# Kernel tuning notes

Measured on AMD Instinct MI355X. Metric: run time of the kernel, lower is better.

The kernel has to match this reference:

```python
import jax, jax.numpy as jnp
import numpy as np

N_NODES, N_EDGES = 1024, 4096
D_NODE, D_EDGE, HEADS, N_CLASSES = 128, 256, 4, 16


def setup_inputs() -> dict:
    key = jax.random.key(0)
    ks = jax.random.split(key, 32)
    def w(i, shape):
        return jax.random.normal(ks[i], shape, dtype=jnp.float32) * 0.02
    inp = {
        'node_features': jax.random.normal(ks[0], (N_NODES, D_NODE), dtype=jnp.float32),
        'edge_features': jax.random.normal(ks[1], (N_EDGES, D_EDGE), dtype=jnp.float32),
        'edge_index': jax.random.randint(ks[2], (2, N_EDGES), 0, N_NODES, dtype=jnp.int32),
    }
    i = 3
    for pre in ('a1', 'a2'):
        for nm, shape in [('Wn', (2 * D_NODE, D_EDGE)), ('Wq', (D_EDGE, D_EDGE)),
                          ('Wk', (D_EDGE, D_EDGE)), ('Wv', (D_EDGE, D_EDGE)), ('Wo', (D_EDGE, D_EDGE))]:
            inp[f'{pre}_{nm}'] = w(i, shape); i += 1
            inp[f'{pre}_b{nm[1:].lower()}'] = jnp.zeros((shape[1],), jnp.float32)
    inp['cls_W1'] = w(i, (D_EDGE, D_EDGE)); i += 1
    inp['cls_b1'] = jnp.zeros((D_EDGE,), jnp.float32)
    inp['cls_W2'] = w(i, (D_EDGE, N_CLASSES)); i += 1
    inp['cls_b2'] = jnp.zeros((N_CLASSES,), jnp.float32)
    return inp


def _edge_adjacency(edge_index):
    # edges adjacent iff they share an endpoint (hops=1). [E,E] bool
    src, dst = edge_index[0], edge_index[1]
    return ((src[:, None] == src[None, :]) | (src[:, None] == dst[None, :]) |
            (dst[:, None] == src[None, :]) | (dst[:, None] == dst[None, :]))


def _edge_attention(ef, nf, edge_index, adj, Wn, bn, Wq, bq, Wk, bk, Wv, bv, Wo, bo):
    src, dst = edge_index[0], edge_index[1]
    # gather endpoint node features and fuse into edge representation
    ctx = jnp.concatenate([nf[src], nf[dst]], axis=-1) @ Wn + bn  # [E, D_EDGE]
    x = ef + ctx
    E, D = x.shape
    hd = D // HEADS
    q = (x @ Wq + bq).reshape(E, HEADS, hd)
    k = (x @ Wk + bk).reshape(E, HEADS, hd)
    v = (x @ Wv + bv).reshape(E, HEADS, hd)
    scores = jnp.einsum('ehd,fhd->hef', q, k) / np.float32(np.sqrt(hd))  # [H,E,E]
    scores = jnp.where(adj[None, :, :], scores, jnp.float32(-1e9))
    attn = jax.nn.softmax(scores, axis=-1)
    out = jnp.einsum('hef,fhd->ehd', attn, v).reshape(E, D)
    return x + out @ Wo + bo


def reference(node_features, edge_features, edge_index,
              a1_Wn, a1_bn, a1_Wq, a1_bq, a1_Wk, a1_bk, a1_Wv, a1_bv, a1_Wo, a1_bo,
              a2_Wn, a2_bn, a2_Wq, a2_bq, a2_Wk, a2_bk, a2_Wv, a2_bv, a2_Wo, a2_bo,
              cls_W1, cls_b1, cls_W2, cls_b2):
    adj = _edge_adjacency(edge_index)
    ef = _edge_attention(edge_features, node_features, edge_index, adj,
                         a1_Wn, a1_bn, a1_Wq, a1_bq, a1_Wk, a1_bk, a1_Wv, a1_bv, a1_Wo, a1_bo)
    ef = _edge_attention(ef, node_features, edge_index, adj,
                         a2_Wn, a2_bn, a2_Wq, a2_bq, a2_Wk, a2_bk, a2_Wv, a2_bv, a2_Wo, a2_bo)
    h = jax.nn.gelu(ef @ cls_W1 + cls_b1, approximate=False)
    return h @ cls_W2 + cls_b2
```

## Files before the change

kernel.cpp:

```cpp
#include <hip/hip_runtime.h>
#include <math.h>

#define E_EDGES 4096
#define N_NODES 1024
#define D_NODE 128
#define D_EDGE 256
#define HEADS 4
#define HD 64
#define N_CLASSES 16
#define CAP 128

typedef __attribute__((ext_vector_type(8))) short short8v;
typedef __attribute__((ext_vector_type(4))) float f32x4;

__device__ __forceinline__ unsigned short f2bf(float f) {
    unsigned u = __float_as_uint(f);
    return (unsigned short)((u + 0x7FFFu + ((u >> 16) & 1u)) >> 16);
}
__device__ __forceinline__ float bf2f(unsigned short b) {
    return __uint_as_float(((unsigned)b) << 16);
}

__device__ __forceinline__ void gload_lds16(const void* g, void* l) {
    __builtin_amdgcn_global_load_lds((const __attribute__((address_space(1))) void*)g,
                                     (__attribute__((address_space(3))) void*)l, 16, 0, 0);
}

__device__ __forceinline__ void xcd_remap(int& bx, int& by)
{
    const int nx = gridDim.x;
    const int lid = blockIdx.x + nx * blockIdx.y;
    const int g = lid & 7, s = lid >> 3;
    const int ppx = gridDim.y >> 3;
    by = g * ppx + s / nx;
    bx = s % nx;
}

__global__ __launch_bounds__(256) void prep(
    const float* W0, const float* W1, const float* W2, const float* W3,
    const float* W4, const float* W5, const float* W6, const float* W7,
    const float* W8, const float* W9, const float* W10,
    short* hiT, short* loT,
    const int* __restrict__ src, const int* __restrict__ dst,
    int* __restrict__ cand, int* __restrict__ ccount)
{
    __shared__ float tl[64][65];
    const int t = threadIdx.x;
    if (blockIdx.x < 176) {
        const float* Ws[11] = {W0, W1, W2, W3, W4, W5, W6, W7, W8, W9, W10};
        const int mat = blockIdx.x >> 4, tile = blockIdx.x & 15;
        const int k0 = (tile >> 2) * 64, n0 = (tile & 3) * 64;
        const float* W = Ws[mat];
#pragma unroll
        for (int p = 0; p < 4; ++p) {
            const int kr = (t >> 4) + p * 16;
            const int nc = (t & 15) * 4;
            *(float4*)&tl[kr][nc] = *(const float4*)&W[(size_t)(k0 + kr) * 256 + n0 + nc];
        }
        __syncthreads();
        const int n = t >> 2, ks = (t & 3) * 16;
        short8v h0, h1, l0, l1;
#pragma unroll
        for (int j = 0; j < 8; ++j) {
            const float x = tl[ks + j][n];
            const unsigned short hb = f2bf(x);
            h0[j] = (short)hb; l0[j] = (short)f2bf(x - bf2f(hb));
        }
#pragma unroll
        for (int j = 0; j < 8; ++j) {
            const float x = tl[ks + 8 + j][n];
            const unsigned short hb = f2bf(x);
            h1[j] = (short)hb; l1[j] = (short)f2bf(x - bf2f(hb));
        }
        short* ho = hiT + (size_t)mat * 65536;
        short* lo = loT + (size_t)mat * 65536;
        *(short8v*)&ho[(size_t)(n0 + n) * 256 + k0 + ks] = h0;
        *(short8v*)&ho[(size_t)(n0 + n) * 256 + k0 + ks + 8] = h1;
        *(short8v*)&lo[(size_t)(n0 + n) * 256 + k0 + ks] = l0;
        *(short8v*)&lo[(size_t)(n0 + n) * 256 + k0 + ks + 8] = l1;
    } else {
        const int w = t >> 6, lane = t & 63;
        const int e = (blockIdx.x - 176) * 4 + w;
        const int a = src[e], b = dst[e];
        int* my = cand + (size_t)e * CAP;
        int base = 0;
        for (int c0 = 0; c0 < E_EDGES; c0 += 64) {
            const int f = c0 + lane;
            const int sf = src[f], df = dst[f];
            const bool adj = (sf == a) | (sf == b) | (df == a) | (df == b);
            const unsigned long long mk = __ballot(adj);
            if (adj) {
                const int pos = base + __popcll(mk & ((1ull << lane) - 1ull));
                if (pos < CAP) my[pos] = f;
            }
            base += __popcll(mk);
        }
        if (lane == 0) ccount[e] = (base < CAP) ? base : CAP;
    }
}

__device__ __forceinline__ void gemm_mfma_core(
    const float* __restrict__ A, const float* __restrict__ A2,
    const short* __restrict__ BhiT, const short* __restrict__ BloT,
    const float* __restrict__ bias, const float* __restrict__ residual,
    const float* __restrict__ residual2, float* __restrict__ C,
    int m0, int n0,
    const float* __restrict__ nf, const int* __restrict__ src,
    const int* __restrict__ dst, int act)
{
    __shared__ short AsH[2][64 * 40];
    __shared__ short AsL[2][64 * 40];
    __shared__ short BsH[2][64 * 32];
    __shared__ short BsL[2][64 * 32];
    const int t = threadIdx.x;
    const int w = t >> 6, lane = t & 63, lr = lane & 15, lg = lane >> 4;
    const int WR = (w >> 1) * 32, WC = (w & 1) * 32;
    const int am = t >> 2, akc = (t & 3) * 8;
    const int bn = t >> 2, bkc = (t & 3) * 8;

    int nS = 0, nD = 0;
    if (nf) { nS = src[m0 + am]; nD = dst[m0 + am]; }

    f32x4 acc00 = {0.f, 0.f, 0.f, 0.f};
    f32x4 acc01 = acc00, acc10 = acc00, acc11 = acc00;
    float4 av0, av1;

#define LOADA_REG(k0)                                                          \
    do {                                                                       \
        const int kq0 = (k0) + akc, kq1 = kq0 + 4;                             \
        if (nf) {                                                              \
            const float* p0 = (kq0 < D_NODE)                                   \
                ? &nf[(size_t)nS * D_NODE + kq0]                               \
                : &nf[(size_t)nD * D_NODE + kq0 - D_NODE];                     \
            const float* p1 = (kq1 < D_NODE)                                   \
                ? &nf[(size_t)nS * D_NODE + kq1]                               \
                : &nf[(size_t)nD * D_NODE + kq1 - D_NODE];                     \
            av0 = *(const float4*)p0; av1 = *(const float4*)p1;                \
        } else {                                                               \
            av0 = *(const float4*)&A[(size_t)(m0 + am) * 256 + kq0];           \
            av1 = *(const float4*)&A[(size_t)(m0 + am) * 256 + kq1];           \
            if (A2) {                                                          \
                const float4 c0_ = *(const float4*)&A2[(size_t)(m0 + am) * 256 + kq0]; \
                const float4 c1_ = *(const float4*)&A2[(size_t)(m0 + am) * 256 + kq1]; \
                av0.x += c0_.x; av0.y += c0_.y; av0.z += c0_.z; av0.w += c0_.w; \
                av1.x += c1_.x; av1.y += c1_.y; av1.z += c1_.z; av1.w += c1_.w; \
            }                                                                  \
        }                                                                      \
    } while (0)
#define SPLIT1(f, j)                                                           \
    { const unsigned short hb = f2bf(f); ah[j] = (short)hb;                    \
      al[j] = (short)f2bf((f) - bf2f(hb)); }
#define STOREA_SPLIT(buf)                                                      \
    do {                                                                       \
        short8v ah, al;                                                        \
        SPLIT1(av0.x, 0) SPLIT1(av0.y, 1) SPLIT1(av0.z, 2) SPLIT1(av0.w, 3)    \
        SPLIT1(av1.x, 4) SPLIT1(av1.y, 5) SPLIT1(av1.z, 6) SPLIT1(av1.w, 7)    \
        *(short8v*)&AsH[buf][am * 40 + akc] = ah;                              \
        *(short8v*)&AsL[buf][am * 40 + akc] = al;                              \
    } while (0)
#define STAGE_B(buf, k0)                                                       \
    do {                                                                       \
        gload_lds16(&BhiT[(size_t)(n0 + bn) * 256 + (k0) + bkc],               \
                    (short*)&BsH[buf][0] + t * 8);                             \
        gload_lds16(&BloT[(size_t)(n0 + bn) * 256 + (k0) + bkc],               \
                    (short*)&BsL[buf][0] + t * 8);                             \
    } while (0)
#define MFMA_STEP(buf)                                                         \
    do {                                                                       \
        const int c0 = WC + lr, c1 = WC + 16 + lr;                             \
        const short8v bH0 = *(const short8v*)&BsH[buf][c0 * 32 + lg * 8];      \
        const short8v bL0 = *(const short8v*)&BsL[buf][c0 * 32 + lg * 8];      \
        const short8v bH1 = *(const short8v*)&BsH[buf][c1 * 32 + lg * 8];      \
        const short8v bL1 = *(const short8v*)&BsL[buf][c1 * 32 + lg * 8];      \
        const short8v aH0 = *(const short8v*)&AsH[buf][(WR + lr) * 40 + lg * 8];      \
        const short8v aL0 = *(const short8v*)&AsL[buf][(WR + lr) * 40 + lg * 8];      \
        const short8v aH1 = *(const short8v*)&AsH[buf][(WR + 16 + lr) * 40 + lg * 8]; \
        const short8v aL1 = *(const short8v*)&AsL[buf][(WR + 16 + lr) * 40 + lg * 8]; \
        acc00 = __builtin_amdgcn_mfma_f32_16x16x32_bf16(aH0, bH0, acc00, 0, 0, 0);    \
        acc01 = __builtin_amdgcn_mfma_f32_16x16x32_bf16(aH0, bH1, acc01, 0, 0, 0);    \
        acc10 = __builtin_amdgcn_mfma_f32_16x16x32_bf16(aH1, bH0, acc10, 0, 0, 0);    \
        acc11 = __builtin_amdgcn_mfma_f32_16x16x32_bf16(aH1, bH1, acc11, 0, 0, 0);    \
        acc00 = __builtin_amdgcn_mfma_f32_16x16x32_bf16(aH0, bL0, acc00, 0, 0, 0);    \
        acc01 = __builtin_amdgcn_mfma_f32_16x16x32_bf16(aH0, bL1, acc01, 0, 0, 0);    \
        acc10 = __builtin_amdgcn_mfma_f32_16x16x32_bf16(aH1, bL0, acc10, 0, 0, 0);    \
        acc11 = __builtin_amdgcn_mfma_f32_16x16x32_bf16(aH1, bL1, acc11, 0, 0, 0);    \
        acc00 = __builtin_amdgcn_mfma_f32_16x16x32_bf16(aL0, bH0, acc00, 0, 0, 0);    \
        acc01 = __builtin_amdgcn_mfma_f32_16x16x32_bf16(aL0, bH1, acc01, 0, 0, 0);    \
        acc10 = __builtin_amdgcn_mfma_f32_16x16x32_bf16(aL1, bH0, acc10, 0, 0, 0);    \
        acc11 = __builtin_amdgcn_mfma_f32_16x16x32_bf16(aL1, bH1, acc11, 0, 0, 0);    \
    } while (0)

    LOADA_REG(0);
    STAGE_B(0, 0);
    STOREA_SPLIT(0);
    __syncthreads();

    for (int kt = 0; kt < 8; ++kt) {
        const int cur = kt & 1;
        if (kt < 7) {
            STAGE_B(cur ^ 1, (kt + 1) * 32);
            LOADA_REG((kt + 1) * 32);
        }
        MFMA_STEP(cur);
        if (kt < 7) STOREA_SPLIT(cur ^ 1);
        __syncthreads();
    }

#define EPI(accv, rt, ct)                                                      \
    do {                                                                       \
        const int col = n0 + WC + (ct) * 16 + lr;                              \
        const float bb = bias ? bias[col] : 0.f;                               \
        _Pragma("unroll") for (int i = 0; i < 4; ++i) {                        \
            const int row = m0 + WR + (rt) * 16 + lg * 4 + i;                  \
            float v = accv[i] + bb;                                            \
            if (residual) v += residual[(size_t)row * D_EDGE + col];           \
            if (residual2) v += residual2[(size_t)row * D_EDGE + col];         \
            if (act == 1) v = 0.5f * v * (1.f + erff(v * 0.70710678118654752f)); \
            C[(size_t)row * D_EDGE + col] = v;                                 \
        }                                                                      \
    } while (0)
    EPI(acc00, 0, 0); EPI(acc01, 0, 1); EPI(acc10, 1, 0); EPI(acc11, 1, 1);
#undef LOADA_REG
#undef SPLIT1
#undef STOREA_SPLIT
#undef STAGE_B
#undef MFMA_STEP
#undef EPI
}

__global__ __launch_bounds__(256) void gemm_ctx(
    const float* __restrict__ nf, const int* __restrict__ src,
    const int* __restrict__ dst, const short* __restrict__ whiT,
    const short* __restrict__ wloT, const float* __restrict__ bn1,
    const float* __restrict__ bn2, float* __restrict__ ctx)
{
    int bx = blockIdx.x, by = blockIdx.y;
    xcd_remap(bx, by);
    const int Lyr = by >> 6, rb = by & 63;
    const short* BH = whiT + (size_t)(Lyr * 5) * 65536;
    const short* BL = wloT + (size_t)(Lyr * 5) * 65536;
    gemm_mfma_core(nullptr, nullptr, BH, BL, Lyr ? bn2 : bn1,
                   nullptr, nullptr, ctx + (size_t)Lyr * E_EDGES * D_EDGE,
                   rb * 64, bx * 64, nf, src, dst, 0);
}

__global__ __launch_bounds__(256) void gemm_mfma(
    const float* __restrict__ A, const float* __restrict__ A2,
    const short* __restrict__ BhiT, const short* __restrict__ BloT,
    const float* __restrict__ bias, const float* __restrict__ residual,
    const float* __restrict__ residual2, float* __restrict__ C, int act)
{
    int bx = blockIdx.x, by = blockIdx.y;
    xcd_remap(bx, by);
    gemm_mfma_core(A, A2, BhiT, BloT, bias, residual, residual2, C,
                   by * 64, bx * 64, nullptr, nullptr, nullptr, act);
}

__global__ __launch_bounds__(256) void gemm_mfma_qkv(
    const float* __restrict__ ef_in, const float* __restrict__ ctx,
    const short* __restrict__ whiT, const short* __restrict__ wloT,
    const float* __restrict__ bq, const float* __restrict__ bk,
    const float* __restrict__ bv,
    float* __restrict__ qb, float* __restrict__ kb, float* __restrict__ vb,
    int wbase)
{
    int bx = blockIdx.x, by = blockIdx.y;
    xcd_remap(bx, by);
    const int wsel = bx >> 2, nt = bx & 3;
    const short* BH = whiT + (size_t)(wbase + 1 + wsel) * 65536;
    const short* BL = wloT + (size_t)(wbase + 1 + wsel) * 65536;
    const float* bias = (wsel == 0) ? bq : (wsel == 1) ? bk : bv;
    float* C = (wsel == 0) ? qb : (wsel == 1) ? kb : vb;
    gemm_mfma_core(ef_in, ctx, BH, BL, bias, nullptr, nullptr, C,
                   by * 64, nt * 64, nullptr, nullptr, nullptr, 0);
}

__global__ __launch_bounds__(256) void attn_sparse4(
    const float* __restrict__ q, const float* __restrict__ k,
    const float* __restrict__ v, const int* __restrict__ cand,
    const int* __restrict__ ccount, float* __restrict__ out)
{
    __shared__ int lc[CAP];
    const int e = blockIdx.x;
    const int t = threadIdx.x, h = t >> 6, lane = t & 63;
    const int g = lane >> 4, il = lane & 15;
    const int m = ccount[e];
    if (t < m) lc[t] = cand[(size_t)e * CAP + t];
    __syncthreads();

    const float4 q4 = *(const float4*)&q[(size_t)e * D_EDGE + h * HD + il * 4];
    float M = -1e30f, L = 0.f;
    float4 O = make_float4(0.f, 0.f, 0.f, 0.f);

    for (int i0 = g; i0 < m; i0 += 8) {
        const int f0 = lc[i0];
        const bool ok1 = (i0 + 4) < m;
        const int f1 = ok1 ? lc[i0 + 4] : f0;
        const float4 k0 = *(const float4*)&k[(size_t)f0 * D_EDGE + h * HD + il * 4];
        const float4 v0 = *(const float4*)&v[(size_t)f0 * D_EDGE + h * HD + il * 4];
        const float4 k1 = *(const float4*)&k[(size_t)f1 * D_EDGE + h * HD + il * 4];
        const float4 v1 = *(const float4*)&v[(size_t)f1 * D_EDGE + h * HD + il * 4];
        float s0 = q4.x * k0.x + q4.y * k0.y + q4.z * k0.z + q4.w * k0.w;
        float s1 = q4.x * k1.x + q4.y * k1.y + q4.z * k1.z + q4.w * k1.w;
        s0 += __shfl_xor(s0, 1); s1 += __shfl_xor(s1, 1);
        s0 += __shfl_xor(s0, 2); s1 += __shfl_xor(s1, 2);
        s0 += __shfl_xor(s0, 4); s1 += __shfl_xor(s1, 4);
        s0 += __shfl_xor(s0, 8); s1 += __shfl_xor(s1, 8);
        s0 *= 0.125f;
        s1 = ok1 ? s1 * 0.125f : -1e30f;
        const float Mn = fmaxf(M, fmaxf(s0, s1));
        const float al = __expf(M - Mn);
        const float p0 = __expf(s0 - Mn), p1 = __expf(s1 - Mn);
        O.x = O.x * al + p0 * v0.x + p1 * v1.x;
        O.y = O.y * al + p0 * v0.y + p1 * v1.y;
        O.z = O.z * al + p0 * v0.z + p1 * v1.z;
        O.w = O.w * al + p0 * v0.w + p1 * v1.w;
        L = L * al + p0 + p1;
        M = Mn;
    }
    float Mo = fmaxf(M, __shfl_xor(M, 16));
    Mo = fmaxf(Mo, __shfl_xor(Mo, 32));
    const float sc = __expf(M - Mo);
    O.x *= sc; O.y *= sc; O.z *= sc; O.w *= sc; L *= sc;
    O.x += __shfl_xor(O.x, 16); O.y += __shfl_xor(O.y, 16);
    O.z += __shfl_xor(O.z, 16); O.w += __shfl_xor(O.w, 16);
    L += __shfl_xor(L, 16);
    O.x += __shfl_xor(O.x, 32); O.y += __shfl_xor(O.y, 32);
    O.z += __shfl_xor(O.z, 32); O.w += __shfl_xor(O.w, 32);
    L += __shfl_xor(L, 32);
    if (lane < 16) {
        const float invL = 1.f / L;
        float4 r = make_float4(O.x * invL, O.y * invL, O.z * invL, O.w * invL);
        *(float4*)&out[(size_t)e * D_EDGE + h * HD + il * 4] = r;
    }
}

__global__ __launch_bounds__(256) void gemm_cls(
    const float* __restrict__ y, const short* __restrict__ BhiT,
    const short* __restrict__ BloT, const float* __restrict__ b1,
    const float* __restrict__ W2, const float* __restrict__ b2,
    float* __restrict__ outp)
{
    __shared__ __attribute__((aligned(16))) char smem[35840];
    short* AsH = (short*)smem;
    short* AsL = (short*)(smem + 1280);
    short* BsH = (short*)(smem + 2560);
    short* BsL = (short*)(smem + 18944);
    short* hH  = (short*)smem;
    short* hL  = (short*)(smem + 8448);
    float* W2s = (float*)(smem + 16896);

    const int t = threadIdx.x;
    const int w = t >> 6, lane = t & 63, lr = lane & 15, lg = lane >> 4;
    const int m0 = blockIdx.x * 16;

    f32x4 acc[4];
#pragma unroll
    for (int ct = 0; ct < 4; ++ct) acc[ct] = (f32x4){0.f, 0.f, 0.f, 0.f};

    for (int kt = 0; kt < 8; ++kt) {
        const int k0 = kt * 32;
        if (t < 128) {
            const int row = t >> 3, kc = (t & 7) * 4;
            const float4 a4 = *(const float4*)&y[(size_t)(m0 + row) * 256 + k0 + kc];
            const float fv[4] = {a4.x, a4.y, a4.z, a4.w};
#pragma unroll
            for (int j = 0; j < 4; ++j) {
                const unsigned short hb = f2bf(fv[j]);
                AsH[row * 40 + kc + j] = (short)hb;
                AsL[row * 40 + kc + j] = (short)f2bf(fv[j] - bf2f(hb));
            }
        }
#pragma unroll
        for (int p = 0; p < 4; ++p) {
            const int idx = t + 256 * p;
            const int n = idx >> 2, k8 = (idx & 3) * 8;
            gload_lds16(&BhiT[(size_t)n * 256 + k0 + k8], BsH + (size_t)idx * 8);
            gload_lds16(&BloT[(size_t)n * 256 + k0 + k8], BsL + (size_t)idx * 8);
        }
        __syncthreads();
        const short8v aH = *(const short8v*)&AsH[lr * 40 + lg * 8];
        const short8v aL = *(const short8v*)&AsL[lr * 40 + lg * 8];
#pragma unroll
        for (int ct = 0; ct < 4; ++ct) {
            const int c = w * 64 + ct * 16 + lr;
            const short8v bH = *(const short8v*)&BsH[c * 32 + lg * 8];
            const short8v bL = *(const short8v*)&BsL[c * 32 + lg * 8];
            acc[ct] = __builtin_amdgcn_mfma_f32_16x16x32_bf16(aH, bH, acc[ct], 0, 0, 0);
            acc[ct] = __builtin_amdgcn_mfma_f32_16x16x32_bf16(aH, bL, acc[ct], 0, 0, 0);
            acc[ct] = __builtin_amdgcn_mfma_f32_16x16x32_bf16(aL, bH, acc[ct], 0, 0, 0);
        }
        __syncthreads();
    }

#pragma unroll
    for (int ct = 0; ct < 4; ++ct) {
        const int col = w * 64 + ct * 16 + lr;
        const float bb = b1[col];
#pragma unroll
        for (int i = 0; i < 4; ++i) {
            const int row = lg * 4 + i;
            float vv = acc[ct][i] + bb;
            vv = 0.5f * vv * (1.f + erff(vv * 0.70710678118654752f));
            const unsigned short hb = f2bf(vv);
            hH[row * 264 + col] = (short)hb;
            hL[row * 264 + col] = (short)f2bf(vv - bf2f(hb));
        }
    }
#pragma unroll
    for (int p = 0; p < 4; ++p) {
        const int idx = t + 256 * p;
        gload_lds16(&W2[(size_t)idx * 4], W2s + (size_t)idx * 4);
    }
    __syncthreads();

    f32x4 o = {0.f, 0.f, 0.f, 0.f};
#pragma unroll
    for (int kk = 0; kk < 8; ++kk) {
        const short8v aH = *(const short8v*)&hH[lr * 264 + kk * 32 + lg * 8];
        const short8v aL = *(const short8v*)&hL[lr * 264 + kk * 32 + lg * 8];
        short8v bH, bL;
#pragma unroll
        for (int j = 0; j < 8; ++j) {
            const float x = W2s[(size_t)(kk * 32 + lg * 8 + j) * 16 + lr];
            const unsigned short hb = f2bf(x);
            bH[j] = (short)hb; bL[j] = (short)f2bf(x - bf2f(hb));
        }
        o = __builtin_amdgcn_mfma_f32_16x16x32_bf16(aH, bH, o, 0, 0, 0);
        o = __builtin_amdgcn_mfma_f32_16x16x32_bf16(aH, bL, o, 0, 0, 0);
        o = __builtin_amdgcn_mfma_f32_16x16x32_bf16(aL, bH, o, 0, 0, 0);
    }
    if (w == 0) {
#pragma unroll
        for (int i = 0; i < 4; ++i) {
            const int row = m0 + lg * 4 + i;
            outp[(size_t)row * 16 + lr] = o[i] + b2[lr];
        }
    }
}

extern "C" void kernel_launch(void* const* d_in, const int* in_sizes, int n_in,
                              void* d_out, int out_size, void* d_ws, size_t ws_size,
                              hipStream_t stream)
{
    const float* nf = (const float*)d_in[0];
    const float* ef = (const float*)d_in[1];
    const int* ei = (const int*)d_in[2];
    const int* src = ei;
    const int* dst = ei + E_EDGES;

    const float* a_Wn[2] = {(const float*)d_in[3],  (const float*)d_in[13]};
    const float* a_bn[2] = {(const float*)d_in[4],  (const float*)d_in[14]};
    const float* a_Wq[2] = {(const float*)d_in[5],  (const float*)d_in[15]};
    const float* a_bq[2] = {(const float*)d_in[6],  (const float*)d_in[16]};
    const float* a_Wk[2] = {(const float*)d_in[7],  (const float*)d_in[17]};
    const float* a_bk[2] = {(const float*)d_in[8],  (const float*)d_in[18]};
    const float* a_Wv[2] = {(const float*)d_in[9],  (const float*)d_in[19]};
    const float* a_bv[2] = {(const float*)d_in[10], (const float*)d_in[20]};
    const float* a_Wo[2] = {(const float*)d_in[11], (const float*)d_in[21]};
    const float* a_bo[2] = {(const float*)d_in[12], (const float*)d_in[22]};
    const float* cls_W1 = (const float*)d_in[23];
    const float* cls_b1 = (const float*)d_in[24];
    const float* cls_W2 = (const float*)d_in[25];
    const float* cls_b2 = (const float*)d_in[26];

    const size_t buf = (size_t)E_EDGES * D_EDGE;
    float* ws = (float*)d_ws;
    float* ctx1 = ws + 0 * buf;
    float* ctx2 = ws + 1 * buf;
    float* qb   = ws + 2 * buf;
    float* kb   = ws + 3 * buf;
    float* vb   = ws + 4 * buf;
    float* ao   = ws + 5 * buf;
    float* y1   = ws + 6 * buf;
    float* y2   = ctx1;
    int* cand   = (int*)(ws + 7 * buf);
    int* ccount = cand + (size_t)E_EDGES * CAP;
    short* whiT = (short*)(ccount + E_EDGES);
    short* wloT = whiT + (size_t)11 * 65536;

    const dim3 gGemm(D_EDGE / 64, E_EDGES / 64);
    const dim3 gCtx(D_EDGE / 64, 2 * E_EDGES / 64);
    const dim3 gQkv(12, E_EDGES / 64);

    prep<<<176 + E_EDGES / 4, 256, 0, stream>>>(
        a_Wn[0], a_Wq[0], a_Wk[0], a_Wv[0], a_Wo[0],
        a_Wn[1], a_Wq[1], a_Wk[1], a_Wv[1], a_Wo[1],
        cls_W1, whiT, wloT, src, dst, cand, ccount);

    gemm_ctx<<<gCtx, 256, 0, stream>>>(nf, src, dst, whiT, wloT,
                                       a_bn[0], a_bn[1], ctx1);

    const float* ef_in = ef;
    const float* ctxL[2] = {ctx1, ctx2};
    float* yout[2] = {y1, y2};
    for (int L = 0; L < 2; ++L) {
        const int wbase = L * 5;
        gemm_mfma_qkv<<<gQkv, 256, 0, stream>>>(
            ef_in, ctxL[L], whiT, wloT, a_bq[L], a_bk[L], a_bv[L],
            qb, kb, vb, wbase);
        attn_sparse4<<<E_EDGES, 256, 0, stream>>>(qb, kb, vb, cand, ccount, ao);
        gemm_mfma<<<gGemm, 256, 0, stream>>>(
            ao, nullptr, whiT + (size_t)(wbase + 4) * 65536,
            wloT + (size_t)(wbase + 4) * 65536,
            a_bo[L], ef_in, ctxL[L], yout[L], 0);
        ef_in = yout[L];
    }

    gemm_cls<<<E_EDGES / 16, 256, 0, stream>>>(
        y2, whiT + (size_t)10 * 65536, wloT + (size_t)10 * 65536,
        cls_b1, cls_W2, cls_b2, (float*)d_out);
}
```

Before: 135.9 us.

## Halve GEMM row tiles to 32 and move adjacency build into ctx kernel

```diff
diff --git a/kernel.cpp b/kernel.cpp
--- a/kernel.cpp
+++ b/kernel.cpp
@@ -11,6 +11,7 @@
 #define CAP 128
 
 typedef __attribute__((ext_vector_type(8))) short short8v;
+typedef __attribute__((ext_vector_type(4))) short short4v;
 typedef __attribute__((ext_vector_type(4))) float f32x4;
 
 __device__ __forceinline__ unsigned short f2bf(float f) {
@@ -24,139 +25,100 @@
 __device__ __forceinline__ void gload_lds16(const void* g, void* l) {
     __builtin_amdgcn_global_load_lds((const __attribute__((address_space(1))) void*)g,
                                      (__attribute__((address_space(3))) void*)l, 16, 0, 0);
-}
-
-__device__ __forceinline__ void xcd_remap(int& bx, int& by)
-{
-    const int nx = gridDim.x;
-    const int lid = blockIdx.x + nx * blockIdx.y;
-    const int g = lid & 7, s = lid >> 3;
-    const int ppx = gridDim.y >> 3;
-    by = g * ppx + s / nx;
-    bx = s % nx;
 }
 
 __global__ __launch_bounds__(256) void prep(
     const float* W0, const float* W1, const float* W2, const float* W3,
     const float* W4, const float* W5, const float* W6, const float* W7,
     const float* W8, const float* W9, const float* W10,
-    short* hiT, short* loT,
-    const int* __restrict__ src, const int* __restrict__ dst,
-    int* __restrict__ cand, int* __restrict__ ccount)
+    short* hiT, short* loT)
 {
     __shared__ float tl[64][65];
     const int t = threadIdx.x;
-    if (blockIdx.x < 176) {
-        const float* Ws[11] = {W0, W1, W2, W3, W4, W5, W6, W7, W8, W9, W10};
-        const int mat = blockIdx.x >> 4, tile = blockIdx.x & 15;
-        const int k0 = (tile >> 2) * 64, n0 = (tile & 3) * 64;
-        const float* W = Ws[mat];
-#pragma unroll
-        for (int p = 0; p < 4; ++p) {
-            const int kr = (t >> 4) + p * 16;
-            const int nc = (t & 15) * 4;
-            *(float4*)&tl[kr][nc] = *(const float4*)&W[(size_t)(k0 + kr) * 256 + n0 + nc];
-        }
-        __syncthreads();
-        const int n = t >> 2, ks = (t & 3) * 16;
-        short8v h0, h1, l0, l1;
-#pragma unroll
-        for (int j = 0; j < 8; ++j) {
-            const float x = tl[ks + j][n];
-            const unsigned short hb = f2bf(x);
-            h0[j] = (short)hb; l0[j] = (short)f2bf(x - bf2f(hb));
-        }
-#pragma unroll
-        for (int j = 0; j < 8; ++j) {
-            const float x = tl[ks + 8 + j][n];
-            const unsigned short hb = f2bf(x);
-            h1[j] = (short)hb; l1[j] = (short)f2bf(x - bf2f(hb));
-        }
-        short* ho = hiT + (size_t)mat * 65536;
-        short* lo = loT + (size_t)mat * 65536;
-        *(short8v*)&ho[(size_t)(n0 + n) * 256 + k0 + ks] = h0;
-        *(short8v*)&ho[(size_t)(n0 + n) * 256 + k0 + ks + 8] = h1;
-        *(short8v*)&lo[(size_t)(n0 + n) * 256 + k0 + ks] = l0;
-        *(short8v*)&lo[(size_t)(n0 + n) * 256 + k0 + ks + 8] = l1;
-    } else {
-        const int w = t >> 6, lane = t & 63;
-        const int e = (blockIdx.x - 176) * 4 + w;
-        const int a = src[e], b = dst[e];
-        int* my = cand + (size_t)e * CAP;
-        int base = 0;
-        for (int c0 = 0; c0 < E_EDGES; c0 += 64) {
-            const int f = c0 + lane;
-            const int sf = src[f], df = dst[f];
-            const bool adj = (sf == a) | (sf == b) | (df == a) | (df == b);
-            const unsigned long long mk = __ballot(adj);
-            if (adj) {
-                const int pos = base + __popcll(mk & ((1ull << lane) - 1ull));
-                if (pos < CAP) my[pos] = f;
-            }
-            base += __popcll(mk);
-        }
-        if (lane == 0) ccount[e] = (base < CAP) ? base : CAP;
-    }
-}
-
-__device__ __forceinline__ void gemm_mfma_core(
+    const float* Ws[11] = {W0, W1, W2, W3, W4, W5, W6, W7, W8, W9, W10};
+    const int mat = blockIdx.x >> 4, tile = blockIdx.x & 15;
+    const int k0 = (tile >> 2) * 64, n0 = (tile & 3) * 64;
+    const float* W = Ws[mat];
+#pragma unroll
+    for (int p = 0; p < 4; ++p) {
+        const int kr = (t >> 4) + p * 16;
+        const int nc = (t & 15) * 4;
+        *(float4*)&tl[kr][nc] = *(const float4*)&W[(size_t)(k0 + kr) * 256 + n0 + nc];
+    }
+    __syncthreads();
+    const int n = t >> 2, ks = (t & 3) * 16;
+    short8v h0, h1, l0, l1;
+#pragma unroll
+    for (int j = 0; j < 8; ++j) {
+        const float x = tl[ks + j][n];
+        const unsigned short hb = f2bf(x);
+        h0[j] = (short)hb; l0[j] = (short)f2bf(x - bf2f(hb));
+    }
+#pragma unroll
+    for (int j = 0; j < 8; ++j) {
+        const float x = tl[ks + 8 + j][n];
+        const unsigned short hb = f2bf(x);
+        h1[j] = (short)hb; l1[j] = (short)f2bf(x - bf2f(hb));
+    }
+    short* ho = hiT + (size_t)mat * 65536;
+    short* lo = loT + (size_t)mat * 65536;
+    *(short8v*)&ho[(size_t)(n0 + n) * 256 + k0 + ks] = h0;
+    *(short8v*)&ho[(size_t)(n0 + n) * 256 + k0 + ks + 8] = h1;
+    *(short8v*)&lo[(size_t)(n0 + n) * 256 + k0 + ks] = l0;
+    *(short8v*)&lo[(size_t)(n0 + n) * 256 + k0 + ks + 8] = l1;
+}
+
+__device__ __forceinline__ void mcore32(
     const float* __restrict__ A, const float* __restrict__ A2,
     const short* __restrict__ BhiT, const short* __restrict__ BloT,
-    const float* __restrict__ bias, const float* __restrict__ residual,
-    const float* __restrict__ residual2, float* __restrict__ C,
+    const float* __restrict__ bias, const float* __restrict__ res,
+    const float* __restrict__ res2, float* __restrict__ C,
     int m0, int n0,
     const float* __restrict__ nf, const int* __restrict__ src,
     const int* __restrict__ dst, int act)
 {
-    __shared__ short AsH[2][64 * 40];
-    __shared__ short AsL[2][64 * 40];
+    __shared__ short AsH[2][32 * 40];
+    __shared__ short AsL[2][32 * 40];
     __shared__ short BsH[2][64 * 32];
     __shared__ short BsL[2][64 * 32];
     const int t = threadIdx.x;
     const int w = t >> 6, lane = t & 63, lr = lane & 15, lg = lane >> 4;
-    const int WR = (w >> 1) * 32, WC = (w & 1) * 32;
-    const int am = t >> 2, akc = (t & 3) * 8;
+    const int WR = (w >> 1) * 16, WC = (w & 1) * 32;
+    const int ar = t >> 3, akc = (t & 7) * 4;
     const int bn = t >> 2, bkc = (t & 3) * 8;
 
     int nS = 0, nD = 0;
-    if (nf) { nS = src[m0 + am]; nD = dst[m0 + am]; }
-
-    f32x4 acc00 = {0.f, 0.f, 0.f, 0.f};
-    f32x4 acc01 = acc00, acc10 = acc00, acc11 = acc00;
-    float4 av0, av1;
-
-#define LOADA_REG(k0)                                                          \
+    if (nf) { nS = src[m0 + ar]; nD = dst[m0 + ar]; }
+
+    f32x4 acc0 = {0.f, 0.f, 0.f, 0.f}, acc1 = {0.f, 0.f, 0.f, 0.f};
+    float4 av;
+
+#define LOADA_R(k0)                                                            \
     do {                                                                       \
-        const int kq0 = (k0) + akc, kq1 = kq0 + 4;                             \
+        const int kq = (k0) + akc;                                             \
         if (nf) {                                                              \
-            const float* p0 = (kq0 < D_NODE)                                   \
-                ? &nf[(size_t)nS * D_NODE + kq0]                               \
-                : &nf[(size_t)nD * D_NODE + kq0 - D_NODE];                     \
-            const float* p1 = (kq1 < D_NODE)                                   \
-                ? &nf[(size_t)nS * D_NODE + kq1]                               \
-                : &nf[(size_t)nD * D_NODE + kq1 - D_NODE];                     \
-            av0 = *(const float4*)p0; av1 = *(const float4*)p1;                \
+            const float* pp = (kq < D_NODE)                                    \
+                ? &nf[(size_t)nS * D_NODE + kq]                                \
+                : &nf[(size_t)nD * D_NODE + kq - D_NODE];                      \
+            av = *(const float4*)pp;                                           \
         } else {                                                               \
-            av0 = *(const float4*)&A[(size_t)(m0 + am) * 256 + kq0];           \
-            av1 = *(const float4*)&A[(size_t)(m0 + am) * 256 + kq1];           \
+            av = *(const float4*)&A[(size_t)(m0 + ar) * 256 + kq];             \
             if (A2) {                                                          \
-                const float4 c0_ = *(const float4*)&A2[(size_t)(m0 + am) * 256 + kq0]; \
-                const float4 c1_ = *(const float4*)&A2[(size_t)(m0 + am) * 256 + kq1]; \
-                av0.x += c0_.x; av0.y += c0_.y; av0.z += c0_.z; av0.w += c0_.w; \
-                av1.x += c1_.x; av1.y += c1_.y; av1.z += c1_.z; av1.w += c1_.w; \
+                const float4 c_ = *(const float4*)&A2[(size_t)(m0 + ar) * 256 + kq]; \
+                av.x += c_.x; av.y += c_.y; av.z += c_.z; av.w += c_.w;        \
             }                                                                  \
         }                                                                      \
     } while (0)
-#define SPLIT1(f, j)                                                           \
-    { const unsigned short hb = f2bf(f); ah[j] = (short)hb;                    \
-      al[j] = (short)f2bf((f) - bf2f(hb)); }
-#define STOREA_SPLIT(buf)                                                      \
+#define STOREA_S(buf)                                                          \
     do {                                                                       \
-        short8v ah, al;                                                        \
-        SPLIT1(av0.x, 0) SPLIT1(av0.y, 1) SPLIT1(av0.z, 2) SPLIT1(av0.w, 3)    \
-        SPLIT1(av1.x, 4) SPLIT1(av1.y, 5) SPLIT1(av1.z, 6) SPLIT1(av1.w, 7)    \
-        *(short8v*)&AsH[buf][am * 40 + akc] = ah;                              \
-        *(short8v*)&AsL[buf][am * 40 + akc] = al;                              \
+        short4v ah, al;                                                        \
+        const float fv[4] = {av.x, av.y, av.z, av.w};                          \
+        _Pragma("unroll") for (int j = 0; j < 4; ++j) {                        \
+            const unsigned short hb = f2bf(fv[j]);                             \
+            ah[j] = (short)hb; al[j] = (short)f2bf(fv[j] - bf2f(hb));          \
+        }                                                                      \
+        *(short4v*)&AsH[buf][ar * 40 + akc] = ah;                              \
+        *(short4v*)&AsL[buf][ar * 40 + akc] = al;                              \
     } while (0)
 #define STAGE_B(buf, k0)                                                       \
     do {                                                                       \
@@ -172,91 +134,96 @@
         const short8v bL0 = *(const short8v*)&BsL[buf][c0 * 32 + lg * 8];      \
         const short8v bH1 = *(const short8v*)&BsH[buf][c1 * 32 + lg * 8];      \
         const short8v bL1 = *(const short8v*)&BsL[buf][c1 * 32 + lg * 8];      \
-        const short8v aH0 = *(const short8v*)&AsH[buf][(WR + lr) * 40 + lg * 8];      \
-        const short8v aL0 = *(const short8v*)&AsL[buf][(WR + lr) * 40 + lg * 8];      \
-        const short8v aH1 = *(const short8v*)&AsH[buf][(WR + 16 + lr) * 40 + lg * 8]; \
-        const short8v aL1 = *(const short8v*)&AsL[buf][(WR + 16 + lr) * 40 + lg * 8]; \
-        acc00 = __builtin_amdgcn_mfma_f32_16x16x32_bf16(aH0, bH0, acc00, 0, 0, 0);    \
-        acc01 = __builtin_amdgcn_mfma_f32_16x16x32_bf16(aH0, bH1, acc01, 0, 0, 0);    \
-        acc10 = __builtin_amdgcn_mfma_f32_16x16x32_bf16(aH1, bH0, acc10, 0, 0, 0);    \
-        acc11 = __builtin_amdgcn_mfma_f32_16x16x32_bf16(aH1, bH1, acc11, 0, 0, 0);    \
-        acc00 = __builtin_amdgcn_mfma_f32_16x16x32_bf16(aH0, bL0, acc00, 0, 0, 0);    \
-        acc01 = __builtin_amdgcn_mfma_f32_16x16x32_bf16(aH0, bL1, acc01, 0, 0, 0);    \
-        acc10 = __builtin_amdgcn_mfma_f32_16x16x32_bf16(aH1, bL0, acc10, 0, 0, 0);    \
-        acc11 = __builtin_amdgcn_mfma_f32_16x16x32_bf16(aH1, bL1, acc11, 0, 0, 0);    \
-        acc00 = __builtin_amdgcn_mfma_f32_16x16x32_bf16(aL0, bH0, acc00, 0, 0, 0);    \
-        acc01 = __builtin_amdgcn_mfma_f32_16x16x32_bf16(aL0, bH1, acc01, 0, 0, 0);    \
-        acc10 = __builtin_amdgcn_mfma_f32_16x16x32_bf16(aL1, bH0, acc10, 0, 0, 0);    \
-        acc11 = __builtin_amdgcn_mfma_f32_16x16x32_bf16(aL1, bH1, acc11, 0, 0, 0);    \
+        const short8v aH = *(const short8v*)&AsH[buf][(WR + lr) * 40 + lg * 8];\
+        const short8v aL = *(const short8v*)&AsL[buf][(WR + lr) * 40 + lg * 8];\
+        acc0 = __builtin_amdgcn_mfma_f32_16x16x32_bf16(aH, bH0, acc0, 0, 0, 0);\
+        acc1 = __builtin_amdgcn_mfma_f32_16x16x32_bf16(aH, bH1, acc1, 0, 0, 0);\
+        acc0 = __builtin_amdgcn_mfma_f32_16x16x32_bf16(aH, bL0, acc0, 0, 0, 0);\
+        acc1 = __builtin_amdgcn_mfma_f32_16x16x32_bf16(aH, bL1, acc1, 0, 0, 0);\
+        acc0 = __builtin_amdgcn_mfma_f32_16x16x32_bf16(aL, bH0, acc0, 0, 0, 0);\
+        acc1 = __builtin_amdgcn_mfma_f32_16x16x32_bf16(aL, bH1, acc1, 0, 0, 0);\
     } while (0)
 
-    LOADA_REG(0);
+    LOADA_R(0);
     STAGE_B(0, 0);
-    STOREA_SPLIT(0);
+    STOREA_S(0);
     __syncthreads();
 
     for (int kt = 0; kt < 8; ++kt) {
         const int cur = kt & 1;
         if (kt < 7) {
             STAGE_B(cur ^ 1, (kt + 1) * 32);
-            LOADA_REG((kt + 1) * 32);
+            LOADA_R((kt + 1) * 32);
         }
         MFMA_STEP(cur);
-        if (kt < 7) STOREA_SPLIT(cur ^ 1);
+        if (kt < 7) STOREA_S(cur ^ 1);
         __syncthreads();
     }
 
-#define EPI(accv, rt, ct)                                                      \
+#define EPI(accv, ct)                                                          \
     do {                                                                       \
         const int col = n0 + WC + (ct) * 16 + lr;                              \
         const float bb = bias ? bias[col] : 0.f;                               \
         _Pragma("unroll") for (int i = 0; i < 4; ++i) {                        \
-            const int row = m0 + WR + (rt) * 16 + lg * 4 + i;                  \
+            const int row = m0 + WR + lg * 4 + i;                              \
             float v = accv[i] + bb;                                            \
-            if (residual) v += residual[(size_t)row * D_EDGE + col];           \
-            if (residual2) v += residual2[(size_t)row * D_EDGE + col];         \
+            if (res)  v += res[(size_t)row * D_EDGE + col];                    \
+            if (res2) v += res2[(size_t)row * D_EDGE + col];                   \
             if (act == 1) v = 0.5f * v * (1.f + erff(v * 0.70710678118654752f)); \
             C[(size_t)row * D_EDGE + col] = v;                                 \
         }                                                                      \
     } while (0)
-    EPI(acc00, 0, 0); EPI(acc01, 0, 1); EPI(acc10, 1, 0); EPI(acc11, 1, 1);
-#undef LOADA_REG
-#undef SPLIT1
-#undef STOREA_SPLIT
+    EPI(acc0, 0); EPI(acc1, 1);
+#undef LOADA_R
+#undef STOREA_S
 #undef STAGE_B
 #undef MFMA_STEP
 #undef EPI
 }
 
-__global__ __launch_bounds__(256) void gemm_ctx(
+__global__ __launch_bounds__(256) void ctx_adj(
     const float* __restrict__ nf, const int* __restrict__ src,
     const int* __restrict__ dst, const short* __restrict__ whiT,
     const short* __restrict__ wloT, const float* __restrict__ bn1,
-    const float* __restrict__ bn2, float* __restrict__ ctx)
-{
-    int bx = blockIdx.x, by = blockIdx.y;
-    xcd_remap(bx, by);
-    const int Lyr = by >> 6, rb = by & 63;
-    const short* BH = whiT + (size_t)(Lyr * 5) * 65536;
-    const short* BL = wloT + (size_t)(Lyr * 5) * 65536;
-    gemm_mfma_core(nullptr, nullptr, BH, BL, Lyr ? bn2 : bn1,
-                   nullptr, nullptr, ctx + (size_t)Lyr * E_EDGES * D_EDGE,
-                   rb * 64, bx * 64, nf, src, dst, 0);
-}
-
-__global__ __launch_bounds__(256) void gemm_mfma(
-    const float* __restrict__ A, const float* __restrict__ A2,
-    const short* __restrict__ BhiT, const short* __restrict__ BloT,
-    const float* __restrict__ bias, const float* __restrict__ residual,
-    const float* __restrict__ residual2, float* __restrict__ C, int act)
-{
-    int bx = blockIdx.x, by = blockIdx.y;
-    xcd_remap(bx, by);
-    gemm_mfma_core(A, A2, BhiT, BloT, bias, residual, residual2, C,
-                   by * 64, bx * 64, nullptr, nullptr, nullptr, act);
-}
-
-__global__ __launch_bounds__(256) void gemm_mfma_qkv(
+    const float* __restrict__ bn2, float* __restrict__ ctx,
+    int* __restrict__ cand, int* __restrict__ ccount)
+{
+    if (blockIdx.x < 1024) {
+        const int lid = blockIdx.x;
+        const int g = lid & 7, s = lid >> 3;
+        const int rowt = g * 32 + (s >> 2);
+        const int ct = s & 3;
+        const int R = rowt * 32;
+        const int Lyr = R >> 12;
+        const int r = R & (E_EDGES - 1);
+        mcore32(nullptr, nullptr,
+                whiT + (size_t)(Lyr * 5) * 65536, wloT + (size_t)(Lyr * 5) * 65536,
+                Lyr ? bn2 : bn1, nullptr, nullptr,
+                ctx + (size_t)Lyr * E_EDGES * D_EDGE,
+                r, ct * 64, nf, src, dst, 0);
+    } else {
+        const int t = threadIdx.x;
+        const int w = t >> 6, lane = t & 63;
+        const int e = (blockIdx.x - 1024) * 4 + w;
+        const int a = src[e], b = dst[e];
+        int* my = cand + (size_t)e * CAP;
+        int base = 0;
+        for (int c0 = 0; c0 < E_EDGES; c0 += 64) {
+            const int f = c0 + lane;
+            const int sf = src[f], df = dst[f];
+            const bool adj = (sf == a) | (sf == b) | (df == a) | (df == b);
+            const unsigned long long mk = __ballot(adj);
+            if (adj) {
+                const int pos = base + __popcll(mk & ((1ull << lane) - 1ull));
+                if (pos < CAP) my[pos] = f;
+            }
+            base += __popcll(mk);
+        }
+        if (lane == 0) ccount[e] = (base < CAP) ? base : CAP;
+    }
+}
+
+__global__ __launch_bounds__(256) void gemm_qkv32(
     const float* __restrict__ ef_in, const float* __restrict__ ctx,
     const short* __restrict__ whiT, const short* __restrict__ wloT,
     const float* __restrict__ bq, const float* __restrict__ bk,
@@ -264,15 +231,30 @@
     float* __restrict__ qb, float* __restrict__ kb, float* __restrict__ vb,
     int wbase)
 {
-    int bx = blockIdx.x, by = blockIdx.y;
-    xcd_remap(bx, by);
-    const int wsel = bx >> 2, nt = bx & 3;
+    const int lid = blockIdx.x;
+    const int g = lid & 7, s = lid >> 3;
+    const int rowt = g * 16 + s / 12;
+    const int rem = s % 12, wsel = rem >> 2, ct = rem & 3;
     const short* BH = whiT + (size_t)(wbase + 1 + wsel) * 65536;
     const short* BL = wloT + (size_t)(wbase + 1 + wsel) * 65536;
     const float* bias = (wsel == 0) ? bq : (wsel == 1) ? bk : bv;
     float* C = (wsel == 0) ? qb : (wsel == 1) ? kb : vb;
-    gemm_mfma_core(ef_in, ctx, BH, BL, bias, nullptr, nullptr, C,
-                   by * 64, nt * 64, nullptr, nullptr, nullptr, 0);
+    mcore32(ef_in, ctx, BH, BL, bias, nullptr, nullptr, C,
+            rowt * 32, ct * 64, nullptr, nullptr, nullptr, 0);
+}
+
+__global__ __launch_bounds__(256) void gemm_wo32(
+    const float* __restrict__ ao, const short* __restrict__ BhiT,
+    const short* __restrict__ BloT, const float* __restrict__ bo,
+    const float* __restrict__ ef_in, const float* __restrict__ ctx,
+    float* __restrict__ y)
+{
+    const int lid = blockIdx.x;
+    const int g = lid & 7, s = lid >> 3;
+    const int rowt = g * 16 + (s >> 2);
+    const int ct = s & 3;
+    mcore32(ao, nullptr, BhiT, BloT, bo, ef_in, ctx, y,
+            rowt * 32, ct * 64, nullptr, nullptr, nullptr, 0);
 }
 
 __global__ __launch_bounds__(256) void attn_sparse4(
@@ -479,31 +461,27 @@
     short* whiT = (short*)(ccount + E_EDGES);
     short* wloT = whiT + (size_t)11 * 65536;
 
-    const dim3 gGemm(D_EDGE / 64, E_EDGES / 64);
-    const dim3 gCtx(D_EDGE / 64, 2 * E_EDGES / 64);
-    const dim3 gQkv(12, E_EDGES / 64);
-
-    prep<<<176 + E_EDGES / 4, 256, 0, stream>>>(
+    prep<<<176, 256, 0, stream>>>(
         a_Wn[0], a_Wq[0], a_Wk[0], a_Wv[0], a_Wo[0],
         a_Wn[1], a_Wq[1], a_Wk[1], a_Wv[1], a_Wo[1],
-        cls_W1, whiT, wloT, src, dst, cand, ccount);
-
-    gemm_ctx<<<gCtx, 256, 0, stream>>>(nf, src, dst, whiT, wloT,
-                                       a_bn[0], a_bn[1], ctx1);
+        cls_W1, whiT, wloT);
+
+    ctx_adj<<<2048, 256, 0, stream>>>(nf, src, dst, whiT, wloT,
+                                      a_bn[0], a_bn[1], ctx1, cand, ccount);
 
     const float* ef_in = ef;
     const float* ctxL[2] = {ctx1, ctx2};
     float* yout[2] = {y1, y2};
     for (int L = 0; L < 2; ++L) {
         const int wbase = L * 5;
-        gemm_mfma_qkv<<<gQkv, 256, 0, stream>>>(
+        gemm_qkv32<<<1536, 256, 0, stream>>>(
             ef_in, ctxL[L], whiT, wloT, a_bq[L], a_bk[L], a_bv[L],
             qb, kb, vb, wbase);
         attn_sparse4<<<E_EDGES, 256, 0, stream>>>(qb, kb, vb, cand, ccount, ao);
-        gemm_mfma<<<gGemm, 256, 0, stream>>>(
-            ao, nullptr, whiT + (size_t)(wbase + 4) * 65536,
+        gemm_wo32<<<512, 256, 0, stream>>>(
+            ao, whiT + (size_t)(wbase + 4) * 65536,
             wloT + (size_t)(wbase + 4) * 65536,
-            a_bo[L], ef_in, ctxL[L], yout[L], 0);
+            a_bo[L], ef_in, ctxL[L], yout[L]);
         ef_in = yout[L];
     }
 
```

Result: faster. 132.4 us (-2.5%).
